# Kernel tuning notes

Hardware: AMD Instinct MI355X
Metric: run time of the kernel (lower is better)

Reference implementation:

```python
import jax, jax.numpy as jnp
import numpy as np

SLOPE = 25.0  # snntorch surrogate.fast_sigmoid default slope
THR = 1.0
BETA = 0.5
NUM_HEADS = 8

@jax.custom_vjp
def spike(u):
    # forward: heaviside; backward: fast-sigmoid surrogate
    return (u > 0).astype(u.dtype)

def _spike_fwd(u):
    return (u > 0).astype(u.dtype), u

def _spike_bwd(u, g):
    return (g / (SLOPE * jnp.abs(u) + 1.0) ** 2,)

spike.defvjp(_spike_fwd, _spike_bwd)

def lif(inp, mem):
    # snntorch Leaky, reset_mechanism='subtract': reset from previous mem (detached)
    reset = jax.lax.stop_gradient((mem > THR).astype(mem.dtype))
    mem_new = BETA * mem + inp - reset * THR
    spk = spike(mem_new - THR)
    return spk, mem_new

def conv1x1(x, W):
    # nn.Conv2d(C,C,1,bias=False): pure channel matmul
    return jnp.einsum('bihw,oi->bohw', x, W)

def setup_inputs():
    key = jax.random.key(0)
    ks = jax.random.split(key, 5)
    B, C, H, W = 8, 256, 64, 64
    x = jax.random.normal(ks[0], (B, C, H, W), jnp.float32)
    z = jnp.zeros((B, C, H, W), jnp.float32)
    s = 1.0 / np.sqrt(C)
    Wq = jax.random.normal(ks[1], (C, C), jnp.float32) * s
    Wk = jax.random.normal(ks[2], (C, C), jnp.float32) * s
    Wv = jax.random.normal(ks[3], (C, C), jnp.float32) * s
    Wo = jax.random.normal(ks[4], (C, C), jnp.float32) * s
    gamma = jnp.ones((C,), jnp.float32)
    beta_bn = jnp.zeros((C,), jnp.float32)
    return {'x': x, 'q_mem': z, 'k_mem': z, 'v_mem': z,
            'Wq': Wq, 'Wk': Wk, 'Wv': Wv, 'Wo': Wo,
            'gamma': gamma, 'beta_bn': beta_bn}

def reference(x, q_mem, k_mem, v_mem, Wq, Wk, Wv, Wo, gamma, beta_bn):
    B, C, H, W = x.shape
    N = H * W
    hd = C // NUM_HEADS
    scale = hd ** -0.5

    q_spk, q_mem_n = lif(conv1x1(x, Wq), q_mem)
    k_spk, k_mem_n = lif(conv1x1(x, Wk), k_mem)
    v_spk, v_mem_n = lif(conv1x1(x, Wv), v_mem)

    # bipolar spikes in {-1,+1}, reshape to (B, h, N, d)
    def to_heads(s):
        t = (2.0 * s - 1.0).reshape(B, NUM_HEADS, hd, N)
        return jnp.transpose(t, (0, 1, 3, 2))

    q = jax.nn.elu(to_heads(q_spk)) + 1.0
    k = jax.nn.elu(to_heads(k_spk)) + 1.0
    v = to_heads(v_spk)

    kv = jnp.einsum('bhnd,bhne->bhde', k, v)            # (B,h,d,d)
    out = jnp.einsum('bhnd,bhde->bhne', q, kv) * scale  # (B,h,N,d)
    k_sum = jnp.sum(k, axis=2)                          # (B,h,d)
    denom = jnp.einsum('bhnd,bhd->bhn', q, k_sum) + 1e-6
    out = out / denom[..., None]

    out = jnp.transpose(out, (0, 1, 3, 2)).reshape(B, C, H, W)
    out = conv1x1(out, Wo)

    # BatchNorm2d, training mode (biased batch stats), eps=1e-5
    mean = jnp.mean(out, axis=(0, 2, 3), keepdims=True)
    var = jnp.var(out, axis=(0, 2, 3), keepdims=True)
    out = (out - mean) / jnp.sqrt(var + 1e-5)
    out = out * gamma[None, :, None, None] + beta_bn[None, :, None, None]

    return (out, q_mem_n, k_mem_n, v_mem_n)
```

## Files before the change

### kernel.cpp

```cpp
#include <hip/hip_runtime.h>

#define B_ 8
#define C_ 256
#define N_ 4096
#define HD_ 32

#define ALPHA_ 0.36787944117144233f
#define BETAS_ (2.0f - ALPHA_)
#define SCALE_ 0.17677669529663687f

typedef _Float16 f16;
typedef _Float16 f16x8 __attribute__((ext_vector_type(8)));
typedef float f32x4 __attribute__((ext_vector_type(4)));
typedef __attribute__((address_space(3))) f16 lds_f16;

#define MFMA(a,b,c) __builtin_amdgcn_mfma_f32_16x16x32_f16((a),(b),(c),0,0,0)

#define GLDS(g, l) __builtin_amdgcn_global_load_lds( \
    (const __attribute__((address_space(1))) void*)(g), \
    (__attribute__((address_space(3))) void*)(l), 16, 0, 0)

#define DSR(dst, off) asm volatile("ds_read_b128 %0, %1" : "=v"(dst) : "v"(off))

__global__ __launch_bounds__(256) void transpose_split(
    const float* __restrict__ x, f16* __restrict__ XTh, f16* __restrict__ XTl)
{
    __shared__ float tile[32][257];
    int t = threadIdx.x;
    int b = blockIdx.z, i0 = blockIdx.y * 32, n0 = blockIdx.x * 256;
    const float* src = x + ((size_t)b * C_ + i0) * N_ + n0;
    int r = t >> 3, c0 = (t & 7) * 32;
    #pragma unroll
    for (int q = 0; q < 8; ++q) {
        float4 v = *reinterpret_cast<const float4*>(src + (size_t)r * N_ + c0 + q * 4);
        tile[r][c0 + q*4 + 0] = v.x; tile[r][c0 + q*4 + 1] = v.y;
        tile[r][c0 + q*4 + 2] = v.z; tile[r][c0 + q*4 + 3] = v.w;
    }
    __syncthreads();
    size_t ob = ((size_t)b * N_ + n0 + t) * C_ + i0;
    #pragma unroll
    for (int q = 0; q < 4; ++q) {
        f16x8 hv, lv;
        #pragma unroll
        for (int j = 0; j < 8; ++j) {
            float v = tile[q*8 + j][t];
            f16 h = (f16)v;
            hv[j] = h;
            lv[j] = (f16)(v - (float)h);
        }
        *reinterpret_cast<f16x8*>(XTh + ob + q*8) = hv;
        *reinterpret_cast<f16x8*>(XTl + ob + q*8) = lv;
    }
}

__global__ __launch_bounds__(256) void weight_split(
    const float* __restrict__ Wq, const float* __restrict__ Wk,
    const float* __restrict__ Wv, const float* __restrict__ Wo,
    f16* __restrict__ Wch, f16* __restrict__ Wcl)
{
    int idx4 = (blockIdx.x * 256 + threadIdx.x) * 4;
    int o = idx4 >> 8, i = idx4 & 255;
    const float* src = (o < 256) ? (Wq + (size_t)o * 256)
                     : (o < 512) ? (Wk + (size_t)(o - 256) * 256)
                     : (o < 768) ? (Wv + (size_t)(o - 512) * 256)
                                 : (Wo + (size_t)(o - 768) * 256);
    float4 v = *reinterpret_cast<const float4*>(src + i);
    f16 h0 = (f16)v.x, h1 = (f16)v.y, h2 = (f16)v.z, h3 = (f16)v.w;
    f16 hh[4] = { h0, h1, h2, h3 };
    f16 ll[4] = { (f16)(v.x - (float)h0), (f16)(v.y - (float)h1),
                  (f16)(v.z - (float)h2), (f16)(v.w - (float)h3) };
    *reinterpret_cast<uint2*>(Wch + idx4) = *reinterpret_cast<uint2*>(hh);
    *reinterpret_cast<uint2*>(Wcl + idx4) = *reinterpret_cast<uint2*>(ll);
}

template<bool LIF>
__global__ __launch_bounds__(256, 2) void mfma_gemm(
    const f16* __restrict__ Wch, const f16* __restrict__ Wcl,
    const f16* __restrict__ Bh,  const f16* __restrict__ Bl,
    const float* __restrict__ mq, const float* __restrict__ mk2,
    const float* __restrict__ mv,
    float* __restrict__ o0, float* __restrict__ o1, float* __restrict__ o2)
{
    int gid = blockIdx.x;
    int b = gid & 7, slot = gid >> 3;
    int conv, oTi, nt;
    if (LIF) { conv = slot % 3; int rest = slot / 3; oTi = rest & 1; nt = rest >> 1; }
    else     { conv = 0;        oTi = slot & 1;      nt = slot >> 1; }
    int wRow0 = (LIF ? conv * 256 : 768) + oTi * 128;
    int chOut0 = oTi * 128;
    int nT = nt * 128;

    const float* memP = nullptr; float* outP;
    if (LIF) {
        memP = (conv == 0) ? mq : (conv == 1) ? mk2 : mv;
        outP = (conv == 0) ? o0 : (conv == 1) ? o1 : o2;
    } else outP = o0;

    __shared__ __align__(16) f16 smem[2][16384];

    int t = threadIdx.x;
    int wid = t >> 6, lane = t & 63;
    int wm = wid >> 1, wn = wid & 1;
    int lr = lane & 15, g = lane >> 4;

    const f16* g0[8];
    #pragma unroll
    for (int i = 0; i < 8; ++i) {
        int s = i * 256 + t;
        const f16* gp;
        if (s < 512) {
            int r = s >> 2, c = (s & 3) ^ ((r >> 1) & 3);
            gp = Wch + (size_t)(wRow0 + r) * 256 + c * 8;
        } else if (s < 1024) {
            int s2 = s - 512; int r = s2 >> 2, c = (s2 & 3) ^ ((r >> 1) & 3);
            gp = Wcl + (size_t)(wRow0 + r) * 256 + c * 8;
        } else if (s < 1536) {
            int s2 = s - 1024; int r = s2 >> 2, c = (s2 & 3) ^ ((r >> 1) & 3);
            gp = Bh + ((size_t)b * N_ + nT + r) * 256 + c * 8;
        } else {
            int s2 = s - 1536; int r = s2 >> 2, c = (s2 & 3) ^ ((r >> 1) & 3);
            gp = Bl + ((size_t)b * N_ + nT + r) * 256 + c * 8;
        }
        g0[i] = gp;
    }

    unsigned lbase = (unsigned)(size_t)(lds_f16*)&smem[0][0];
    unsigned offAh[4], offAl[4], offBh[4], offBl[4];
    #pragma unroll
    for (int m = 0; m < 4; ++m) {
        int r = wm * 64 + m * 16 + lr;
        int sw = g ^ ((r >> 1) & 3);
        offAh[m] = (unsigned)((r * 4 + sw) * 16);
        offAl[m] = (unsigned)((512 + r * 4 + sw) * 16);
    }
    #pragma unroll
    for (int n = 0; n < 4; ++n) {
        int r = wn * 64 + n * 16 + lr;
        int sw = g ^ ((r >> 1) & 3);
        offBh[n] = (unsigned)((1024 + r * 4 + sw) * 16);
        offBl[n] = (unsigned)((1536 + r * 4 + sw) * 16);
    }

    f32x4 acc[4][4];
    #pragma unroll
    for (int m = 0; m < 4; ++m)
        #pragma unroll
        for (int n = 0; n < 4; ++n) acc[m][n] = (f32x4){0.f, 0.f, 0.f, 0.f};

    #pragma unroll
    for (int i = 0; i < 8; ++i)
        GLDS(g0[i], &smem[0][(i * 256 + t) * 8]);
    __syncthreads();

    #pragma unroll
    for (int ks = 0; ks < 8; ++ks) {
        const int cur = ks & 1;
        if (ks < 7) {
            const int k = (ks + 1) * 32;
            #pragma unroll
            for (int i = 0; i < 8; ++i)
                GLDS(g0[i] + k, &smem[cur ^ 1][(i * 256 + t) * 8]);
        }
        const unsigned base = lbase + (unsigned)(cur * 32768);
        f16x8 ah[4], al[4], bhf[4], blf[4];
        #pragma unroll
        for (int m = 0; m < 4; ++m) { DSR(ah[m], base + offAh[m]); DSR(al[m], base + offAl[m]); }
        #pragma unroll
        for (int n = 0; n < 4; ++n) { DSR(bhf[n], base + offBh[n]); DSR(blf[n], base + offBl[n]); }
        asm volatile("s_waitcnt lgkmcnt(0)" ::: "memory");
        __builtin_amdgcn_sched_barrier(0);
        #pragma unroll
        for (int n = 0; n < 4; ++n)
            #pragma unroll
            for (int m = 0; m < 4; ++m) {
                acc[m][n] = MFMA(ah[m], bhf[n], acc[m][n]);
                acc[m][n] = MFMA(ah[m], blf[n], acc[m][n]);
                acc[m][n] = MFMA(al[m], bhf[n], acc[m][n]);
            }
        __builtin_amdgcn_sched_barrier(0);
        asm volatile("s_waitcnt vmcnt(0)" ::: "memory");
        __builtin_amdgcn_s_barrier();
    }

    #pragma unroll
    for (int m = 0; m < 4; ++m) {
        int oLoc = chOut0 + wm * 64 + m * 16 + g * 4;
        #pragma unroll
        for (int n = 0; n < 4; ++n) {
            int nn = nT + wn * 64 + n * 16 + lr;
            #pragma unroll
            for (int r = 0; r < 4; ++r) {
                size_t idx = ((size_t)b * C_ + oLoc + r) * N_ + nn;
                float v = acc[m][n][r];
                if (LIF) {
                    float mm = memP[idx];
                    outP[idx] = 0.5f * mm + v - (mm > 1.0f ? 1.0f : 0.0f);
                } else {
                    outP[idx] = v;
                }
            }
        }
    }
}

__global__ __launch_bounds__(256) void kv_stage1(
    const float* __restrict__ Km, const float* __restrict__ Vm,
    int* __restrict__ pkv, int* __restrict__ pck, int* __restrict__ pcv)
{
    int bh = blockIdx.x, sl = blockIdx.y;
    int b = bh >> 3, h = bh & 7;
    const float* Kp = Km + ((size_t)(b * C_ + h * HD_)) * N_ + sl * 512;
    const float* Vp = Vm + ((size_t)(b * C_ + h * HD_)) * N_ + sl * 512;

    __shared__ unsigned long long mk[32][9], mv[32][9];
    int t = threadIdx.x, wave = t >> 6, lane = t & 63;

    for (int r = wave; r < 32; r += 4) {
        const float* kr = Kp + (size_t)r * N_;
        const float* vr = Vp + (size_t)r * N_;
        #pragma unroll
        for (int seg = 0; seg < 2; ++seg) {
            float4 kf = *reinterpret_cast<const float4*>(kr + seg * 256 + lane * 4);
            float4 vf = *reinterpret_cast<const float4*>(vr + seg * 256 + lane * 4);
            unsigned long long k0 = __ballot(kf.x > 1.0f);
            unsigned long long k1 = __ballot(kf.y > 1.0f);
            unsigned long long k2 = __ballot(kf.z > 1.0f);
            unsigned long long k3 = __ballot(kf.w > 1.0f);
            unsigned long long v0 = __ballot(vf.x > 1.0f);
            unsigned long long v1 = __ballot(vf.y > 1.0f);
            unsigned long long v2 = __ballot(vf.z > 1.0f);
            unsigned long long v3 = __ballot(vf.w > 1.0f);
            if (lane == 0) {
                mk[r][seg*4+0] = k0; mk[r][seg*4+1] = k1;
                mk[r][seg*4+2] = k2; mk[r][seg*4+3] = k3;
                mv[r][seg*4+0] = v0; mv[r][seg*4+1] = v1;
                mv[r][seg*4+2] = v2; mv[r][seg*4+3] = v3;
            }
        }
    }
    __syncthreads();

    int base = (bh * 8 + sl);
    int d = t >> 3, e0 = (t & 7) * 4;
    #pragma unroll
    for (int j = 0; j < 4; ++j) {
        int e = e0 + j, P = 0;
        #pragma unroll
        for (int w = 0; w < 8; ++w) P += __popcll(mk[d][w] & mv[e][w]);
        pkv[(size_t)base * 1024 + d * 32 + e] = P;
    }
    if (t < 32) {
        int c = 0;
        #pragma unroll
        for (int w = 0; w < 8; ++w) c += __popcll(mk[t][w]);
        pck[base * 32 + t] = c;
    } else if (t < 64) {
        int dd = t - 32, c = 0;
        #pragma unroll
        for (int w = 0; w < 8; ++w) c += __popcll(mv[dd][w]);
        pcv[base * 32 + dd] = c;
    }
}

__global__ __launch_bounds__(256) void kv_stage2(
    const int* __restrict__ pkv, const int* __restrict__ pck,
    const int* __restrict__ pcv, float* __restrict__ kvp, float* __restrict__ ksump)
{
    int bh = blockIdx.x, t = threadIdx.x;
    __shared__ float ck[32], cv[32];
    if (t < 32) {
        int s = 0;
        #pragma unroll
        for (int sl = 0; sl < 8; ++sl) s += pck[(bh * 8 + sl) * 32 + t];
        ck[t] = (float)s;
    } else if (t < 64) {
        int dd = t - 32, s = 0;
        #pragma unroll
        for (int sl = 0; sl < 8; ++sl) s += pcv[(bh * 8 + sl) * 32 + dd];
        cv[dd] = (float)s;
    }
    __syncthreads();
    int d = t >> 3, e0 = (t & 7) * 4;
    #pragma unroll
    for (int j = 0; j < 4; ++j) {
        int e = e0 + j, P = 0;
        #pragma unroll
        for (int sl = 0; sl < 8; ++sl) P += pkv[(size_t)(bh * 8 + sl) * 1024 + d * 32 + e];
        float skv = 2.0f * (float)P - ck[d];
        float sv  = 2.0f * cv[e] - 4096.0f;
        kvp[(size_t)bh * 1024 + d * 32 + e] = ALPHA_ * sv + BETAS_ * skv;
    }
    if ((t & 7) == 0)
        ksump[bh * 32 + d] = ALPHA_ * 4096.0f + BETAS_ * ck[d];
}

__global__ __launch_bounds__(256) void att_kernel(
    const float* __restrict__ Qm, const float* __restrict__ kvp,
    const float* __restrict__ ksump, f16* __restrict__ ATh, f16* __restrict__ ATl)
{
    int bh = blockIdx.y; int b = bh >> 3, h = bh & 7;
    int n0 = blockIdx.x * 256;
    const float* Qp = Qm + ((size_t)(b * C_ + h * HD_)) * N_;

    __shared__ float qs[32][260];
    int t = threadIdx.x;
    {
        int r  = t >> 3, c0 = (t & 7) * 32;
        #pragma unroll
        for (int q4 = 0; q4 < 8; ++q4) {
            float4 v = *reinterpret_cast<const float4*>(&Qp[(size_t)r * N_ + n0 + c0 + q4 * 4]);
            qs[r][c0 + q4*4 + 0] = (v.x > 1.0f) ? 2.0f : ALPHA_;
            qs[r][c0 + q4*4 + 1] = (v.y > 1.0f) ? 2.0f : ALPHA_;
            qs[r][c0 + q4*4 + 2] = (v.z > 1.0f) ? 2.0f : ALPHA_;
            qs[r][c0 + q4*4 + 3] = (v.w > 1.0f) ? 2.0f : ALPHA_;
        }
    }
    __syncthreads();

    float q[32];
    #pragma unroll
    for (int d2 = 0; d2 < 32; ++d2) q[d2] = qs[d2][t];

    const float* ksb = ksump + bh * 32;
    float den = 1e-6f;
    #pragma unroll
    for (int d2 = 0; d2 < 32; ++d2) den += q[d2] * ksb[d2];
    float rden = SCALE_ / den;

    const float* kvb = kvp + (size_t)bh * 1024;
    size_t ob = ((size_t)b * N_ + n0 + t) * C_ + h * HD_;
    #pragma unroll
    for (int qq = 0; qq < 4; ++qq) {
        f16x8 hv, lv;
        #pragma unroll
        for (int j = 0; j < 8; ++j) {
            int e = qq * 8 + j;
            float num = 0.0f;
            #pragma unroll
            for (int d2 = 0; d2 < 32; ++d2) num += q[d2] * kvb[d2 * 32 + e];
            float val = num * rden;
            f16 hh = (f16)val;
            hv[j] = hh;
            lv[j] = (f16)(val - (float)hh);
        }
        *reinterpret_cast<f16x8*>(ATh + ob + qq * 8) = hv;
        *reinterpret_cast<f16x8*>(ATl + ob + qq * 8) = lv;
    }
}

__global__ __launch_bounds__(1024) void bn_stats(
    const float* __restrict__ out2, float* __restrict__ stats)
{
    int o = blockIdx.x, t = threadIdx.x;
    double s = 0.0, ss = 0.0;
    for (int b = 0; b < B_; ++b) {
        const float* p = out2 + ((size_t)b * C_ + o) * N_;
        float4 v = *reinterpret_cast<const float4*>(&p[t * 4]);
        s  += (double)v.x + (double)v.y + (double)v.z + (double)v.w;
        ss += (double)v.x * v.x + (double)v.y * v.y + (double)v.z * v.z + (double)v.w * v.w;
    }
    __shared__ double rs[1024], rss[1024];
    rs[t] = s; rss[t] = ss;
    __syncthreads();
    for (int st = 512; st > 0; st >>= 1) {
        if (t < st) { rs[t] += rs[t + st]; rss[t] += rss[t + st]; }
        __syncthreads();
    }
    if (t == 0) {
        double mean = rs[0] / 32768.0;
        double var  = rss[0] / 32768.0 - mean * mean;
        stats[o * 2 + 0] = (float)mean;
        stats[o * 2 + 1] = (float)(1.0 / sqrt(var + 1e-5));
    }
}

__global__ __launch_bounds__(256) void bn_apply(
    float* __restrict__ out, const float* __restrict__ stats,
    const float* __restrict__ gamma, const float* __restrict__ beta)
{
    size_t i = ((size_t)blockIdx.x * 256 + threadIdx.x) * 4;
    int o = (int)((i >> 12) & 255);
    float m = stats[o * 2], r = stats[o * 2 + 1];
    float g = gamma[o] * r;
    float c = beta[o] - m * g;
    float4 v = *reinterpret_cast<float4*>(&out[i]);
    v.x = v.x * g + c; v.y = v.y * g + c;
    v.z = v.z * g + c; v.w = v.w * g + c;
    *reinterpret_cast<float4*>(&out[i]) = v;
}

extern "C" void kernel_launch(void* const* d_in, const int* in_sizes, int n_in,
                              void* d_out, int out_size, void* d_ws, size_t ws_size,
                              hipStream_t stream)
{
    (void)in_sizes; (void)n_in; (void)out_size; (void)ws_size;

    const float* x     = (const float*)d_in[0];
    const float* qmem  = (const float*)d_in[1];
    const float* kmem  = (const float*)d_in[2];
    const float* vmem  = (const float*)d_in[3];
    const float* Wq    = (const float*)d_in[4];
    const float* Wk    = (const float*)d_in[5];
    const float* Wv    = (const float*)d_in[6];
    const float* Wo    = (const float*)d_in[7];
    const float* gamma = (const float*)d_in[8];
    const float* beta  = (const float*)d_in[9];

    const size_t TSZ = (size_t)B_ * C_ * N_;
    float* out0 = (float*)d_out;
    float* outq = out0 + TSZ;
    float* outk = outq + TSZ;
    float* outv = outk + TSZ;

    char* w = (char*)d_ws;
    f16* XTh = (f16*)w;           w += TSZ * 2;
    f16* XTl = (f16*)w;           w += TSZ * 2;
    f16* ATh = (f16*)w;           w += TSZ * 2;
    f16* ATl = (f16*)w;           w += TSZ * 2;
    f16* Wch = (f16*)w;           w += 1024 * 256 * 2;
    f16* Wcl = (f16*)w;           w += 1024 * 256 * 2;
    int* pkv = (int*)w;           w += 64 * 8 * 1024 * 4;
    int* pck = (int*)w;           w += 64 * 8 * 32 * 4;
    int* pcv = (int*)w;           w += 64 * 8 * 32 * 4;
    float* kvp   = (float*)w;     w += 64 * 1024 * 4;
    float* ksump = (float*)w;     w += 64 * 32 * 4;
    float* stats = (float*)w;     w += 256 * 2 * 4;

    dim3 blk(256);

    transpose_split<<<dim3(16, 8, 8), blk, 0, stream>>>(x, XTh, XTl);
    weight_split<<<dim3(256), blk, 0, stream>>>(Wq, Wk, Wv, Wo, Wch, Wcl);

    mfma_gemm<true><<<dim3(1536), blk, 0, stream>>>(
        Wch, Wcl, XTh, XTl, qmem, kmem, vmem, outq, outk, outv);

    kv_stage1<<<dim3(64, 8), blk, 0, stream>>>(outk, outv, pkv, pck, pcv);
    kv_stage2<<<dim3(64), blk, 0, stream>>>(pkv, pck, pcv, kvp, ksump);

    att_kernel<<<dim3(16, 64), blk, 0, stream>>>(outq, kvp, ksump, ATh, ATl);

    mfma_gemm<false><<<dim3(512), blk, 0, stream>>>(
        Wch, Wcl, ATh, ATl, nullptr, nullptr, nullptr, out0, nullptr, nullptr);

    bn_stats<<<dim3(256), dim3(1024), 0, stream>>>(out0, stats);
    bn_apply<<<dim3(8192), blk, 0, stream>>>(out0, stats, gamma, beta);
}
```

Measured before the change: 179.3 us.

## Drop split-f16 precision for output GEMM and load weights straight from global

```diff
diff --git a/kernel.cpp b/kernel.cpp
--- a/kernel.cpp
+++ b/kernel.cpp
@@ -73,14 +73,17 @@
     *reinterpret_cast<uint2*>(Wcl + idx4) = *reinterpret_cast<uint2*>(ll);
 }
 
-template<bool LIF>
-__global__ __launch_bounds__(256, 2) void mfma_gemm(
+template<bool LIF, bool FULLP>
+__global__ __launch_bounds__(256, 3) void mfma_gemm(
     const f16* __restrict__ Wch, const f16* __restrict__ Wcl,
     const f16* __restrict__ Bh,  const f16* __restrict__ Bl,
     const float* __restrict__ mq, const float* __restrict__ mk2,
     const float* __restrict__ mv,
     float* __restrict__ o0, float* __restrict__ o1, float* __restrict__ o2)
 {
+    constexpr int SLOTS = FULLP ? 1024 : 512;
+    constexpr int NGL   = FULLP ? 4 : 2;
+
     int gid = blockIdx.x;
     int b = gid & 7, slot = gid >> 3;
     int conv, oTi, nt;
@@ -96,49 +99,34 @@
         outP = (conv == 0) ? o0 : (conv == 1) ? o1 : o2;
     } else outP = o0;
 
-    __shared__ __align__(16) f16 smem[2][16384];
+    __shared__ __align__(16) f16 smem[2][SLOTS * 8];
 
     int t = threadIdx.x;
     int wid = t >> 6, lane = t & 63;
     int wm = wid >> 1, wn = wid & 1;
     int lr = lane & 15, g = lane >> 4;
 
-    const f16* g0[8];
-    #pragma unroll
-    for (int i = 0; i < 8; ++i) {
+    const f16* gB[NGL];
+    #pragma unroll
+    for (int i = 0; i < NGL; ++i) {
         int s = i * 256 + t;
-        const f16* gp;
-        if (s < 512) {
-            int r = s >> 2, c = (s & 3) ^ ((r >> 1) & 3);
-            gp = Wch + (size_t)(wRow0 + r) * 256 + c * 8;
-        } else if (s < 1024) {
-            int s2 = s - 512; int r = s2 >> 2, c = (s2 & 3) ^ ((r >> 1) & 3);
-            gp = Wcl + (size_t)(wRow0 + r) * 256 + c * 8;
-        } else if (s < 1536) {
-            int s2 = s - 1024; int r = s2 >> 2, c = (s2 & 3) ^ ((r >> 1) & 3);
-            gp = Bh + ((size_t)b * N_ + nT + r) * 256 + c * 8;
-        } else {
-            int s2 = s - 1536; int r = s2 >> 2, c = (s2 & 3) ^ ((r >> 1) & 3);
-            gp = Bl + ((size_t)b * N_ + nT + r) * 256 + c * 8;
-        }
-        g0[i] = gp;
-    }
+        int sp = s & 511;
+        int r = sp >> 2, c = (sp & 3) ^ ((r >> 1) & 3);
+        const f16* plane = (s < 512) ? Bh : Bl;
+        gB[i] = plane + ((size_t)b * N_ + nT + r) * 256 + c * 8;
+    }
+
+    int aOff[4];
+    #pragma unroll
+    for (int m = 0; m < 4; ++m)
+        aOff[m] = (wRow0 + wm * 64 + m * 16 + lr) * 256 + g * 8;
 
     unsigned lbase = (unsigned)(size_t)(lds_f16*)&smem[0][0];
-    unsigned offAh[4], offAl[4], offBh[4], offBl[4];
-    #pragma unroll
-    for (int m = 0; m < 4; ++m) {
-        int r = wm * 64 + m * 16 + lr;
-        int sw = g ^ ((r >> 1) & 3);
-        offAh[m] = (unsigned)((r * 4 + sw) * 16);
-        offAl[m] = (unsigned)((512 + r * 4 + sw) * 16);
-    }
+    unsigned offB[4];
     #pragma unroll
     for (int n = 0; n < 4; ++n) {
         int r = wn * 64 + n * 16 + lr;
-        int sw = g ^ ((r >> 1) & 3);
-        offBh[n] = (unsigned)((1024 + r * 4 + sw) * 16);
-        offBl[n] = (unsigned)((1536 + r * 4 + sw) * 16);
+        offB[n] = (unsigned)((r * 4 + (g ^ ((r >> 1) & 3))) * 16);
     }
 
     f32x4 acc[4][4];
@@ -148,25 +136,33 @@
         for (int n = 0; n < 4; ++n) acc[m][n] = (f32x4){0.f, 0.f, 0.f, 0.f};
 
     #pragma unroll
-    for (int i = 0; i < 8; ++i)
-        GLDS(g0[i], &smem[0][(i * 256 + t) * 8]);
+    for (int i = 0; i < NGL; ++i)
+        GLDS(gB[i], &smem[0][(i * 256 + t) * 8]);
     __syncthreads();
 
     #pragma unroll
     for (int ks = 0; ks < 8; ++ks) {
         const int cur = ks & 1;
+        const int k0 = ks * 32;
+        f16x8 ah[4], al[4];
+        #pragma unroll
+        for (int m = 0; m < 4; ++m) {
+            ah[m] = *reinterpret_cast<const f16x8*>(Wch + aOff[m] + k0);
+            if (FULLP) al[m] = *reinterpret_cast<const f16x8*>(Wcl + aOff[m] + k0);
+        }
+        __builtin_amdgcn_sched_barrier(0);
         if (ks < 7) {
-            const int k = (ks + 1) * 32;
             #pragma unroll
-            for (int i = 0; i < 8; ++i)
-                GLDS(g0[i] + k, &smem[cur ^ 1][(i * 256 + t) * 8]);
-        }
-        const unsigned base = lbase + (unsigned)(cur * 32768);
-        f16x8 ah[4], al[4], bhf[4], blf[4];
-        #pragma unroll
-        for (int m = 0; m < 4; ++m) { DSR(ah[m], base + offAh[m]); DSR(al[m], base + offAl[m]); }
-        #pragma unroll
-        for (int n = 0; n < 4; ++n) { DSR(bhf[n], base + offBh[n]); DSR(blf[n], base + offBl[n]); }
+            for (int i = 0; i < NGL; ++i)
+                GLDS(gB[i] + k0 + 32, &smem[cur ^ 1][(i * 256 + t) * 8]);
+        }
+        const unsigned base = lbase + (unsigned)(cur * (SLOTS * 16));
+        f16x8 bhf[4], blf[4];
+        #pragma unroll
+        for (int n = 0; n < 4; ++n) {
+            DSR(bhf[n], base + offB[n]);
+            if (FULLP) DSR(blf[n], base + offB[n] + 8192);
+        }
         asm volatile("s_waitcnt lgkmcnt(0)" ::: "memory");
         __builtin_amdgcn_sched_barrier(0);
         #pragma unroll
@@ -174,12 +170,16 @@
             #pragma unroll
             for (int m = 0; m < 4; ++m) {
                 acc[m][n] = MFMA(ah[m], bhf[n], acc[m][n]);
-                acc[m][n] = MFMA(ah[m], blf[n], acc[m][n]);
-                acc[m][n] = MFMA(al[m], bhf[n], acc[m][n]);
+                if (FULLP) {
+                    acc[m][n] = MFMA(ah[m], blf[n], acc[m][n]);
+                    acc[m][n] = MFMA(al[m], bhf[n], acc[m][n]);
+                }
             }
         __builtin_amdgcn_sched_barrier(0);
-        asm volatile("s_waitcnt vmcnt(0)" ::: "memory");
-        __builtin_amdgcn_s_barrier();
+        if (ks < 7) {
+            asm volatile("s_waitcnt vmcnt(0)" ::: "memory");
+            __builtin_amdgcn_s_barrier();
+        }
     }
 
     #pragma unroll
@@ -296,7 +296,7 @@
 
 __global__ __launch_bounds__(256) void att_kernel(
     const float* __restrict__ Qm, const float* __restrict__ kvp,
-    const float* __restrict__ ksump, f16* __restrict__ ATh, f16* __restrict__ ATl)
+    const float* __restrict__ ksump, f16* __restrict__ ATh)
 {
     int bh = blockIdx.y; int b = bh >> 3, h = bh & 7;
     int n0 = blockIdx.x * 256;
@@ -331,20 +331,16 @@
     size_t ob = ((size_t)b * N_ + n0 + t) * C_ + h * HD_;
     #pragma unroll
     for (int qq = 0; qq < 4; ++qq) {
-        f16x8 hv, lv;
+        f16x8 hv;
         #pragma unroll
         for (int j = 0; j < 8; ++j) {
             int e = qq * 8 + j;
             float num = 0.0f;
             #pragma unroll
             for (int d2 = 0; d2 < 32; ++d2) num += q[d2] * kvb[d2 * 32 + e];
-            float val = num * rden;
-            f16 hh = (f16)val;
-            hv[j] = hh;
-            lv[j] = (f16)(val - (float)hh);
+            hv[j] = (f16)(num * rden);
         }
         *reinterpret_cast<f16x8*>(ATh + ob + qq * 8) = hv;
-        *reinterpret_cast<f16x8*>(ATl + ob + qq * 8) = lv;
     }
 }
 
@@ -416,7 +412,6 @@
     f16* XTh = (f16*)w;           w += TSZ * 2;
     f16* XTl = (f16*)w;           w += TSZ * 2;
     f16* ATh = (f16*)w;           w += TSZ * 2;
-    f16* ATl = (f16*)w;           w += TSZ * 2;
     f16* Wch = (f16*)w;           w += 1024 * 256 * 2;
     f16* Wcl = (f16*)w;           w += 1024 * 256 * 2;
     int* pkv = (int*)w;           w += 64 * 8 * 1024 * 4;
@@ -431,16 +426,16 @@
     transpose_split<<<dim3(16, 8, 8), blk, 0, stream>>>(x, XTh, XTl);
     weight_split<<<dim3(256), blk, 0, stream>>>(Wq, Wk, Wv, Wo, Wch, Wcl);
 
-    mfma_gemm<true><<<dim3(1536), blk, 0, stream>>>(
+    mfma_gemm<true, true><<<dim3(1536), blk, 0, stream>>>(
         Wch, Wcl, XTh, XTl, qmem, kmem, vmem, outq, outk, outv);
 
     kv_stage1<<<dim3(64, 8), blk, 0, stream>>>(outk, outv, pkv, pck, pcv);
     kv_stage2<<<dim3(64), blk, 0, stream>>>(pkv, pck, pcv, kvp, ksump);
 
-    att_kernel<<<dim3(16, 64), blk, 0, stream>>>(outq, kvp, ksump, ATh, ATl);
-
-    mfma_gemm<false><<<dim3(512), blk, 0, stream>>>(
-        Wch, Wcl, ATh, ATl, nullptr, nullptr, nullptr, out0, nullptr, nullptr);
+    att_kernel<<<dim3(16, 64), blk, 0, stream>>>(outq, kvp, ksump, ATh);
+
+    mfma_gemm<false, false><<<dim3(512), blk, 0, stream>>>(
+        Wch, Wcl, ATh, ATh, nullptr, nullptr, nullptr, out0, nullptr, nullptr);
 
     bn_stats<<<dim3(256), dim3(1024), 0, stream>>>(out0, stats);
     bn_apply<<<dim3(8192), blk, 0, stream>>>(out0, stats, gamma, beta);
```

Measured after the change: 191.5 us. +6.8%, slower.
